# Kernel optimization log

Measured on AMD Instinct MI355X. Metric: run time of the kernel, lower is better.

Reference implementation:

```python
import jax, jax.numpy as jnp
import numpy as np

D_MODEL = 1024
N_HEADS = 16
HEAD_DIM = D_MODEL // N_HEADS
BASE = 10000.0


def _rope_cos_sin(seq_len):
    # inv_freq: [head_dim/2]
    inv_freq = 1.0 / (BASE ** (jnp.arange(0, HEAD_DIM, 2, dtype=jnp.float32) / HEAD_DIM))
    t = jnp.arange(seq_len, dtype=jnp.float32)
    freqs = jnp.outer(t, inv_freq)                 # [S, head_dim/2]
    emb = jnp.concatenate([freqs, freqs], axis=-1)  # [S, head_dim]
    return jnp.cos(emb), jnp.sin(emb)


def _rotate_half(x):
    x1, x2 = jnp.split(x, 2, axis=-1)
    return jnp.concatenate([-x2, x1], axis=-1)


def setup_inputs() -> dict:
    key = jax.random.key(0)
    ks = jax.random.split(key, 9)
    B, S, D = 2, 2048, D_MODEL
    sc = 1.0 / np.sqrt(D)
    return {
        "x": jax.random.normal(ks[0], (B, S, D), jnp.float32),
        "Wq": jax.random.normal(ks[1], (D, D), jnp.float32) * sc,
        "bq": jax.random.normal(ks[2], (D,), jnp.float32) * 0.01,
        "Wk": jax.random.normal(ks[3], (D, D), jnp.float32) * sc,
        "bk": jax.random.normal(ks[4], (D,), jnp.float32) * 0.01,
        "Wv": jax.random.normal(ks[5], (D, D), jnp.float32) * sc,
        "bv": jax.random.normal(ks[6], (D,), jnp.float32) * 0.01,
        "Wo": jax.random.normal(ks[7], (D, D), jnp.float32) * sc,
        "bo": jax.random.normal(ks[8], (D,), jnp.float32) * 0.01,
    }


def reference(x, Wq, bq, Wk, bk, Wv, bv, Wo, bo):
    B, S, D = x.shape
    H, Hd = N_HEADS, HEAD_DIM
    # projections (torch Linear: x @ W.T + b), reshape to [B, H, S, Hd]
    def proj(W, b):
        y = jnp.einsum('bsd,ed->bse', x, W) + b
        return y.reshape(B, S, H, Hd).transpose(0, 2, 1, 3)
    q, k, v = proj(Wq, bq), proj(Wk, bk), proj(Wv, bv)
    cos, sin = _rope_cos_sin(S)            # [S, Hd]
    cos = cos[None, None]                   # [1,1,S,Hd]
    sin = sin[None, None]
    q = q * cos + _rotate_half(q) * sin
    k = k * cos + _rotate_half(k) * sin
    scale = jnp.sqrt(jnp.float32(Hd))
    scores = jnp.einsum('bhqd,bhkd->bhqk', q, k) / scale  # [B,H,S,S]
    attn = jax.nn.softmax(scores, axis=-1)
    out = jnp.einsum('bhqk,bhkd->bhqd', attn, v)          # [B,H,S,Hd]
    out = out.transpose(0, 2, 1, 3).reshape(B, S, D)
    return jnp.einsum('bsd,ed->bse', out, Wo) + bo
```

## Files before the change

kernel.cpp:

```cpp
#include <hip/hip_runtime.h>
#include <hip/hip_fp16.h>
#include <math.h>

#define D_MODEL 1024
#define NH 16
#define HD 64
#define SEQ 2048
#define BATCH 2
#define MROWS (BATCH*SEQ)
#define KDIM 1024

typedef unsigned short u16;
typedef __attribute__((ext_vector_type(8))) _Float16 h8;
typedef __attribute__((ext_vector_type(8))) short s8v;
typedef __attribute__((ext_vector_type(4))) float f4v;

#define MFMAH(a, b, c) __builtin_amdgcn_mfma_f32_16x16x32_f16(a, b, c, 0, 0, 0)

__device__ __forceinline__ void gld16(const u16* g, u16* l) {
    __builtin_amdgcn_global_load_lds(
        (const __attribute__((address_space(1))) void*)g,
        (__attribute__((address_space(3))) void*)l, 16, 0, 0);
}

__device__ __forceinline__ u16 f32_to_f16(float f) {
    return __half_as_ushort(__float2half(f));
}

__global__ __launch_bounds__(256)
void convert_f16(const float* __restrict__ x,
                 const float* __restrict__ Wq, const float* __restrict__ Wk,
                 const float* __restrict__ Wv, const float* __restrict__ Wo,
                 u16* __restrict__ xF,
                 u16* __restrict__ WqF, u16* __restrict__ WkF,
                 u16* __restrict__ WvF, u16* __restrict__ WoF,
                 float2* __restrict__ ropeT) {
    int i = blockIdx.x * 256 + threadIdx.x;
    if (i >= (1 << 20)) {
        int idx2 = i - (1 << 20);
        int s  = idx2 >> 5;
        int dd = idx2 & 31;
        float inv = __expf(-(float)dd * 0.2878231366f);
        float ang = (float)s * inv;
        ropeT[idx2] = make_float2(cosf(ang), sinf(ang));
        return;
    }
    const float* src;
    u16* dst;
    int idx;
    if (i < (1 << 19)) {
        src = x; dst = xF; idx = i;
    } else {
        int j = i - (1 << 19);
        int w = j >> 17;
        idx = j & ((1 << 17) - 1);
        switch (w) {
            case 0:  src = Wq; dst = WqF; break;
            case 1:  src = Wk; dst = WkF; break;
            case 2:  src = Wv; dst = WvF; break;
            default: src = Wo; dst = WoF; break;
        }
    }
    float4 a = ((const float4*)src)[idx * 2];
    float4 b = ((const float4*)src)[idx * 2 + 1];
    s8v o;
    o[0] = (short)f32_to_f16(a.x); o[1] = (short)f32_to_f16(a.y);
    o[2] = (short)f32_to_f16(a.z); o[3] = (short)f32_to_f16(a.w);
    o[4] = (short)f32_to_f16(b.x); o[5] = (short)f32_to_f16(b.y);
    o[6] = (short)f32_to_f16(b.z); o[7] = (short)f32_to_f16(b.w);
    ((s8v*)dst)[idx] = o;
}

__global__ __launch_bounds__(256, 2)
void qkv_gemm(const u16* __restrict__ xF, const u16* __restrict__ WqF,
              const u16* __restrict__ WkF, const u16* __restrict__ WvF,
              const float* __restrict__ bq, const float* __restrict__ bk,
              const float* __restrict__ bv,
              const float2* __restrict__ ropeT,
              u16* __restrict__ QF, u16* __restrict__ KF,
              u16* __restrict__ VtF, float* __restrict__ km2) {
    __shared__ __align__(16) u16 SMEM[32768];

    const int t    = threadIdx.x;
    const int w    = t >> 6;
    const int lane = t & 63;
    const int quad = lane >> 4;
    const int l15  = lane & 15;
    const int wr   = w >> 1;
    const int wc   = w & 1;

    const int bid  = blockIdx.x;
    const int xcd  = bid & 7;
    const int j    = bid >> 3;
    const int m0   = (xcd * 4 + (j & 3)) * 128;
    const int yt   = j >> 2;
    const int wsel = yt >> 3;
    const int n0   = (yt & 7) * 128;

    const u16* Bg;
    const float* bias;
    if (wsel == 0)      { Bg = WqF; bias = bq; }
    else if (wsel == 1) { Bg = WkF; bias = bk; }
    else                { Bg = WvF; bias = bv; }

    const int lr = lane >> 3;
    const int lc = (((lane & 7) ^ lr)) * 8;

    f4v acc[4][4];
    #pragma unroll
    for (int i = 0; i < 4; i++)
        #pragma unroll
        for (int jj = 0; jj < 4; jj++)
            acc[i][jj] = (f4v){0.f, 0.f, 0.f, 0.f};

#define STAGE(K0, DB) do {                                                   \
    u16* As_ = SMEM + (DB);                                                  \
    u16* Bs_ = As_ + 8192;                                                   \
    _Pragma("unroll")                                                        \
    for (int jj_ = 0; jj_ < 4; jj_++) {                                      \
        int seg = jj_ * 4 + w;                                               \
        gld16(xF + (size_t)(m0 + seg * 8 + lr) * KDIM + (K0) + lc,           \
              As_ + seg * 512);                                              \
        gld16(Bg + (size_t)(n0 + seg * 8 + lr) * KDIM + (K0) + lc,           \
              Bs_ + seg * 512);                                              \
    }                                                                        \
} while (0)

    STAGE(0, 0);
    __syncthreads();

    int buf = 0;
    for (int k0 = 0; k0 < KDIM; k0 += 64) {
        if (k0 + 64 < KDIM) STAGE(k0 + 64, (buf ^ 1) * 16384);

        const u16* As = SMEM + buf * 16384;
        const u16* Bs = As + 8192;
        #pragma unroll
        for (int kk = 0; kk < 2; kk++) {
            const int swz = ((kk * 4 + quad) ^ (l15 & 7)) << 3;
            h8 a[4], b[4];
            #pragma unroll
            for (int mt = 0; mt < 4; mt++)
                a[mt] = *(const h8*)&As[(wr * 64 + mt * 16 + l15) * 64 + swz];
            #pragma unroll
            for (int nt = 0; nt < 4; nt++)
                b[nt] = *(const h8*)&Bs[(wc * 64 + nt * 16 + l15) * 64 + swz];
            #pragma unroll
            for (int mt = 0; mt < 4; mt++)
                #pragma unroll
                for (int nt = 0; nt < 4; nt++)
                    acc[mt][nt] = MFMAH(a[mt], b[nt], acc[mt][nt]);
        }
        __syncthreads();
        buf ^= 1;
    }
#undef STAGE

    const int bb = m0 >> 11;
    const int s0 = m0 & 2047;
    const int h0 = n0 >> 6;

    if (wsel < 2) {
        u16* OF = (wsel == 0) ? QF : KF;
        float kn_max = 0.f;
        #pragma unroll
        for (int mt = 0; mt < 4; mt++) {
            #pragma unroll
            for (int r = 0; r < 4; r++) {
                int R = wr * 64 + mt * 16 + quad * 4 + r;
                int s = s0 + R;
                float rowsum = 0.f;
                #pragma unroll
                for (int nt = 0; nt < 2; nt++) {
                    int col = wc * 64 + nt * 16 + l15;
                    int n1 = n0 + col;
                    int dd = n1 & 31;
                    float v1 = acc[mt][nt][r]     + bias[n1];
                    float v2 = acc[mt][nt + 2][r] + bias[n1 + 32];
                    float2 cssn = ropeT[(s << 5) | dd];
                    float cs  = cssn.x;
                    float sn  = cssn.y;
                    float r1 = v1 * cs - v2 * sn;
                    float r2 = v2 * cs + v1 * sn;
                    rowsum += v1 * v1 + v2 * v2;
                    SMEM[R * 128 + (((col >> 3) ^ (R & 15)) << 3) + (col & 7)]
                        = f32_to_f16(r1);
                    int col2 = col + 32;
                    SMEM[R * 128 + (((col2 >> 3) ^ (R & 15)) << 3) + (col2 & 7)]
                        = f32_to_f16(r2);
                }
                if (wsel == 1) {
                    rowsum += __shfl_xor(rowsum, 1, 64);
                    rowsum += __shfl_xor(rowsum, 2, 64);
                    rowsum += __shfl_xor(rowsum, 4, 64);
                    rowsum += __shfl_xor(rowsum, 8, 64);
                    kn_max = fmaxf(kn_max, rowsum);
                }
            }
        }
        if (wsel == 1) {
            kn_max = fmaxf(kn_max, __shfl_xor(kn_max, 16, 64));
            kn_max = fmaxf(kn_max, __shfl_xor(kn_max, 32, 64));
            if (lane == 0) atomicMax((int*)km2, __float_as_int(kn_max));
        }
        __syncthreads();
        #pragma unroll
        for (int cc = 0; cc < 8; cc++) {
            int idx  = cc * 256 + t;
            int hl   = idx >> 10;
            int rem  = idx & 1023;
            int R    = rem >> 3;
            int dch  = rem & 7;
            s8v val = *(const s8v*)&SMEM[R * 128 +
                          (((hl * 8 + dch) ^ (R & 15)) << 3)];
            *(s8v*)(OF + (((size_t)bb * NH + h0 + hl) * SEQ + s0 + R) * 64
                       + dch * 8) = val;
        }
    } else {
        #pragma unroll
        for (int mt = 0; mt < 4; mt++) {
            #pragma unroll
            for (int nt = 0; nt < 4; nt++) {
                int n = wc * 64 + nt * 16 + l15;
                float bv_ = bias[n0 + n];
                #pragma unroll
                for (int r = 0; r < 4; r++) {
                    int m = wr * 64 + mt * 16 + quad * 4 + r;
                    float v = acc[mt][nt][r] + bv_;
                    SMEM[n * 128 + (((m >> 3) ^ (n & 15)) << 3) + (m & 7)]
                        = f32_to_f16(v);
                }
            }
        }
        __syncthreads();
        #pragma unroll
        for (int cc = 0; cc < 8; cc++) {
            int idx = cc * 256 + t;
            int n   = idx >> 4;
            int mc  = idx & 15;
            int d   = n & 63;
            int hh  = n >> 6;
            size_t obase = ((size_t)((bb * NH + h0 + hh) * HD + d)) * SEQ + s0;
            s8v val = *(const s8v*)&SMEM[n * 128 + ((mc ^ (n & 15)) << 3)];
            *(s8v*)(VtF + obase + mc * 8) = val;
        }
    }
}

__global__ __launch_bounds__(256, 4)
void flash_attn(const u16* __restrict__ QF, const u16* __restrict__ KF,
                const u16* __restrict__ VtF,
                const float* __restrict__ kmax2,
                u16* __restrict__ AOF) {
    __shared__ __align__(16) u16 KS[2][32 * 72];
    __shared__ __align__(16) u16 VtS[2][64 * 40];
    __shared__ __align__(16) u16 PS[64 * 40];

    const int t    = threadIdx.x;
    const int w    = t >> 6;
    const int lane = t & 63;
    const int quad = lane >> 4;
    const int l15  = lane & 15;

    const int bid = blockIdx.x;
    const int xcd = bid & 7;
    const int j   = bid >> 3;
    const int bh  = xcd * 4 + (j & 3);
    const int q0  = (j >> 2) * 64;

    const size_t kvbase = (size_t)bh * SEQ * HD;
    const float km2 = kmax2[0];

    h8 qf[2];
    float mb[4];
    {
        const u16* qp = QF + kvbase +
            (size_t)(q0 + w * 16 + l15) * HD + quad * 8;
        qf[0] = *(const h8*)qp;
        qf[1] = *(const h8*)(qp + 32);
        float qn2 = 0.f;
        #pragma unroll
        for (int st = 0; st < 2; st++)
            #pragma unroll
            for (int e = 0; e < 8; e++) {
                float v = (float)qf[st][e];
                qn2 += v * v;
            }
        qn2 += __shfl_xor(qn2, 16, 64);
        qn2 += __shfl_xor(qn2, 32, 64);
        #pragma unroll
        for (int r = 0; r < 4; r++) {
            int src = (lane & 48) | (quad * 4 + r);
            float qr = __shfl(qn2, src, 64);
            mb[r] = sqrtf(qr * km2) * 0.125f;
        }
    }

    f4v o[4];
    float lsum[4];
    #pragma unroll
    for (int nt = 0; nt < 4; nt++) {
        o[nt] = (f4v){0.f, 0.f, 0.f, 0.f};
        lsum[nt] = 0.f;
    }

    for (int k0 = 0; k0 < SEQ; k0 += 64) {
        __syncthreads();

        {
            int row = t >> 3;
            int dc  = (t & 7) * 8;
            *(s8v*)&KS[0][row * 72 + dc] =
                *(const s8v*)(KF + kvbase + (size_t)(k0 + row) * HD + dc);
            *(s8v*)&KS[1][row * 72 + dc] =
                *(const s8v*)(KF + kvbase + (size_t)(k0 + 32 + row) * HD + dc);
        }
        {
            int d  = t >> 2;
            int kc = (t & 3) * 8;
            size_t g = (size_t)bh * HD * SEQ + (size_t)d * SEQ + k0 + kc;
            int col = kc ^ (((d >> 3) & 3) << 3);
            *(s8v*)&VtS[0][d * 40 + col] = *(const s8v*)(VtF + g);
            *(s8v*)&VtS[1][d * 40 + col] = *(const s8v*)(VtF + g + 32);
        }
        __syncthreads();

        #pragma unroll
        for (int sub = 0; sub < 2; sub++) {
            const u16* kb0 = KS[sub] + l15 * 72 + quad * 8;
            const u16* kb1 = KS[sub] + (16 + l15) * 72 + quad * 8;
            h8 kh0 = *(const h8*)kb0, kh1 = *(const h8*)(kb0 + 32);
            h8 kh2 = *(const h8*)kb1, kh3 = *(const h8*)(kb1 + 32);

            f4v sc0 = (f4v){0.f, 0.f, 0.f, 0.f};
            f4v sc1 = (f4v){0.f, 0.f, 0.f, 0.f};
            sc0 = MFMAH(qf[0], kh0, sc0);
            sc0 = MFMAH(qf[1], kh1, sc0);
            sc1 = MFMAH(qf[0], kh2, sc1);
            sc1 = MFMAH(qf[1], kh3, sc1);

            #pragma unroll
            for (int r = 0; r < 4; r++) {
                float p0 = __expf(sc0[r] * 0.125f - mb[r]);
                float p1 = __expf(sc1[r] * 0.125f - mb[r]);
                lsum[r] += p0 + p1;
                int row_l = w * 16 + quad * 4 + r;
                int cs = row_l & 8;
                PS[row_l * 40 + (l15 ^ cs)]        = f32_to_f16(p0);
                PS[row_l * 40 + ((16 + l15) ^ cs)] = f32_to_f16(p1);
            }

            const int prow = w * 16 + l15;
            h8 ph = *(const h8*)&PS[prow * 40 + ((quad * 8) ^ (prow & 8))];
            #pragma unroll
            for (int nt = 0; nt < 4; nt++) {
                int dim = nt * 16 + l15;
                int voff = dim * 40 + ((quad * 8) ^ (((dim >> 3) & 3) << 3));
                o[nt] = MFMAH(ph, *(const h8*)&VtS[sub][voff], o[nt]);
            }
        }
    }

    const int b = bh >> 4;
    const int h = bh & 15;
    #pragma unroll
    for (int r = 0; r < 4; r++) {
        float l = lsum[r];
        l += __shfl_xor(l, 1, 64);
        l += __shfl_xor(l, 2, 64);
        l += __shfl_xor(l, 4, 64);
        l += __shfl_xor(l, 8, 64);
        float inv_l = 1.0f / l;
        int s = q0 + w * 16 + quad * 4 + r;
        size_t obase = (((size_t)b * SEQ + s) * NH + h) * HD;
        #pragma unroll
        for (int nt = 0; nt < 4; nt++) {
            AOF[obase + nt * 16 + l15] = f32_to_f16(o[nt][r] * inv_l);
        }
    }
}

__global__ __launch_bounds__(256, 2)
void gemm_out(const u16* __restrict__ AF, const u16* __restrict__ BF,
              const float* __restrict__ bias, float* __restrict__ out) {
    __shared__ __align__(16) u16 SMEM[24576];

    const int t    = threadIdx.x;
    const int w    = t >> 6;
    const int lane = t & 63;
    const int quad = lane >> 4;
    const int l15  = lane & 15;
    const int wr   = w >> 1;
    const int wc   = w & 1;

    const int bid = blockIdx.x;
    const int xcd = bid & 7;
    const int j   = bid >> 3;
    const int m0  = (xcd * 4 + (j & 3)) * 128;
    const int n0  = (j >> 2) * 64;

    const int lr = lane >> 3;
    const int lc = (((lane & 7) ^ lr)) * 8;

    f4v acc[4][2];
    #pragma unroll
    for (int i = 0; i < 4; i++)
        #pragma unroll
        for (int jj = 0; jj < 2; jj++)
            acc[i][jj] = (f4v){0.f, 0.f, 0.f, 0.f};

#define STAGE(K0, DB) do {                                                   \
    u16* As_ = SMEM + (DB);                                                  \
    u16* Bs_ = As_ + 8192;                                                   \
    _Pragma("unroll")                                                        \
    for (int jj_ = 0; jj_ < 4; jj_++) {                                      \
        int seg = jj_ * 4 + w;                                               \
        gld16(AF + (size_t)(m0 + seg * 8 + lr) * KDIM + (K0) + lc,           \
              As_ + seg * 512);                                              \
    }                                                                        \
    _Pragma("unroll")                                                        \
    for (int jj_ = 0; jj_ < 2; jj_++) {                                      \
        int seg = jj_ * 4 + w;                                               \
        gld16(BF + (size_t)(n0 + seg * 8 + lr) * KDIM + (K0) + lc,           \
              Bs_ + seg * 512);                                              \
    }                                                                        \
} while (0)

    STAGE(0, 0);
    __syncthreads();

    int buf = 0;
    for (int k0 = 0; k0 < KDIM; k0 += 64) {
        if (k0 + 64 < KDIM) STAGE(k0 + 64, (buf ^ 1) * 12288);

        const u16* As = SMEM + buf * 12288;
        const u16* Bs = As + 8192;
        #pragma unroll
        for (int kk = 0; kk < 2; kk++) {
            const int swz = ((kk * 4 + quad) ^ (l15 & 7)) << 3;
            h8 a[4], b[2];
            #pragma unroll
            for (int mt = 0; mt < 4; mt++)
                a[mt] = *(const h8*)&As[(wr * 64 + mt * 16 + l15) * 64 + swz];
            #pragma unroll
            for (int nt = 0; nt < 2; nt++)
                b[nt] = *(const h8*)&Bs[(wc * 32 + nt * 16 + l15) * 64 + swz];
            #pragma unroll
            for (int mt = 0; mt < 4; mt++)
                #pragma unroll
                for (int nt = 0; nt < 2; nt++)
                    acc[mt][nt] = MFMAH(a[mt], b[nt], acc[mt][nt]);
        }
        __syncthreads();
        buf ^= 1;
    }
#undef STAGE

    #pragma unroll
    for (int mt = 0; mt < 4; mt++) {
        #pragma unroll
        for (int nt = 0; nt < 2; nt++) {
            int n = n0 + wc * 32 + nt * 16 + l15;
            float bv = bias[n];
            #pragma unroll
            for (int r = 0; r < 4; r++) {
                int m = m0 + wr * 64 + mt * 16 + quad * 4 + r;
                out[(size_t)m * 1024 + n] = acc[mt][nt][r] + bv;
            }
        }
    }
}

extern "C" void kernel_launch(void* const* d_in, const int* in_sizes, int n_in,
                              void* d_out, int out_size, void* d_ws, size_t ws_size,
                              hipStream_t stream) {
    const float* x  = (const float*)d_in[0];
    const float* Wq = (const float*)d_in[1];
    const float* bq = (const float*)d_in[2];
    const float* Wk = (const float*)d_in[3];
    const float* bk = (const float*)d_in[4];
    const float* Wv = (const float*)d_in[5];
    const float* bv = (const float*)d_in[6];
    const float* Wo = (const float*)d_in[7];
    const float* bo = (const float*)d_in[8];
    float* out = (float*)d_out;

    const size_t TEN = (size_t)MROWS * KDIM;
    const size_t WSZ = (size_t)KDIM * KDIM;

    u16* xF  = (u16*)d_ws;
    u16* WqF = xF + TEN;
    u16* WkF = WqF + WSZ;
    u16* WvF = WkF + WSZ;
    u16* WoF = WvF + WSZ;
    u16* QF  = WoF + WSZ;
    u16* KF  = QF + TEN;
    u16* VtF = KF + TEN;
    float* km2 = (float*)(VtF + TEN);
    float2* ropeT = (float2*)(km2 + 4);
    u16* AOF = xF;

    convert_f16<<<4352, 256, 0, stream>>>(x, Wq, Wk, Wv, Wo,
                                          xF, WqF, WkF, WvF, WoF, ropeT);

    hipMemsetAsync(km2, 0, 4, stream);

    qkv_gemm<<<768, 256, 0, stream>>>(xF, WqF, WkF, WvF,
                                      bq, bk, bv, ropeT, QF, KF, VtF, km2);

    flash_attn<<<1024, 256, 0, stream>>>(QF, KF, VtF, km2, AOF);

    gemm_out<<<512, 256, 0, stream>>>(AOF, WoF, bo, out);
}
```

Before: 210.6 us.

## Prefetch next K/V tile into registers, raise MFMA priority, repad P buffer

The flash attention loop now issues global loads for the next K and Vt tile into registers right after storing the current tile to shared memory, so global latency overlaps with the current tile's compute. MFMA sections are wrapped in s_setprio to favour matrix issue across waves. The P staging buffer changes from a 40-halfword XOR-swizzled stride to a 36-halfword padded stride. This adds register pressure at 4 waves/SIMD occupancy, and the new P layout may change LDS bank-conflict behaviour for the 16-byte reads.

```diff
diff --git a/kernel.cpp b/kernel.cpp
--- a/kernel.cpp
+++ b/kernel.cpp
@@ -254,7 +254,7 @@
                 u16* __restrict__ AOF) {
     __shared__ __align__(16) u16 KS[2][32 * 72];
     __shared__ __align__(16) u16 VtS[2][64 * 40];
-    __shared__ __align__(16) u16 PS[64 * 40];
+    __shared__ __align__(16) u16 PS[64 * 36];
 
     const int t    = threadIdx.x;
     const int w    = t >> 6;
@@ -304,24 +304,31 @@
         lsum[nt] = 0.f;
     }
 
+    const int krow = t >> 3;
+    const int kdc  = (t & 7) * 8;
+    const u16* kgp = KF + kvbase + (size_t)krow * HD + kdc;
+    const int vd   = t >> 2;
+    const int vkc  = (t & 3) * 8;
+    const int vcol = vkc ^ (((vd >> 3) & 3) << 3);
+    const u16* vgp = VtF + (size_t)bh * HD * SEQ + (size_t)vd * SEQ + vkc;
+
+    s8v krg0 = *(const s8v*)(kgp);
+    s8v krg1 = *(const s8v*)(kgp + (size_t)32 * HD);
+    s8v vrg0 = *(const s8v*)(vgp);
+    s8v vrg1 = *(const s8v*)(vgp + 32);
+
     for (int k0 = 0; k0 < SEQ; k0 += 64) {
         __syncthreads();
-
-        {
-            int row = t >> 3;
-            int dc  = (t & 7) * 8;
-            *(s8v*)&KS[0][row * 72 + dc] =
-                *(const s8v*)(KF + kvbase + (size_t)(k0 + row) * HD + dc);
-            *(s8v*)&KS[1][row * 72 + dc] =
-                *(const s8v*)(KF + kvbase + (size_t)(k0 + 32 + row) * HD + dc);
-        }
-        {
-            int d  = t >> 2;
-            int kc = (t & 3) * 8;
-            size_t g = (size_t)bh * HD * SEQ + (size_t)d * SEQ + k0 + kc;
-            int col = kc ^ (((d >> 3) & 3) << 3);
-            *(s8v*)&VtS[0][d * 40 + col] = *(const s8v*)(VtF + g);
-            *(s8v*)&VtS[1][d * 40 + col] = *(const s8v*)(VtF + g + 32);
+        *(s8v*)&KS[0][krow * 72 + kdc] = krg0;
+        *(s8v*)&KS[1][krow * 72 + kdc] = krg1;
+        *(s8v*)&VtS[0][vd * 40 + vcol] = vrg0;
+        *(s8v*)&VtS[1][vd * 40 + vcol] = vrg1;
+        if (k0 + 64 < SEQ) {
+            const u16* kn = kgp + (size_t)(k0 + 64) * HD;
+            krg0 = *(const s8v*)(kn);
+            krg1 = *(const s8v*)(kn + (size_t)32 * HD);
+            vrg0 = *(const s8v*)(vgp + k0 + 64);
+            vrg1 = *(const s8v*)(vgp + k0 + 96);
         }
         __syncthreads();
 
@@ -334,10 +341,12 @@
 
             f4v sc0 = (f4v){0.f, 0.f, 0.f, 0.f};
             f4v sc1 = (f4v){0.f, 0.f, 0.f, 0.f};
+            __builtin_amdgcn_s_setprio(1);
             sc0 = MFMAH(qf[0], kh0, sc0);
             sc0 = MFMAH(qf[1], kh1, sc0);
             sc1 = MFMAH(qf[0], kh2, sc1);
             sc1 = MFMAH(qf[1], kh3, sc1);
+            __builtin_amdgcn_s_setprio(0);
 
             #pragma unroll
             for (int r = 0; r < 4; r++) {
@@ -345,19 +354,20 @@
                 float p1 = __expf(sc1[r] * 0.125f - mb[r]);
                 lsum[r] += p0 + p1;
                 int row_l = w * 16 + quad * 4 + r;
-                int cs = row_l & 8;
-                PS[row_l * 40 + (l15 ^ cs)]        = f32_to_f16(p0);
-                PS[row_l * 40 + ((16 + l15) ^ cs)] = f32_to_f16(p1);
+                PS[row_l * 36 + l15]      = f32_to_f16(p0);
+                PS[row_l * 36 + 16 + l15] = f32_to_f16(p1);
             }
 
             const int prow = w * 16 + l15;
-            h8 ph = *(const h8*)&PS[prow * 40 + ((quad * 8) ^ (prow & 8))];
+            h8 ph = *(const h8*)&PS[prow * 36 + quad * 8];
+            __builtin_amdgcn_s_setprio(1);
             #pragma unroll
             for (int nt = 0; nt < 4; nt++) {
                 int dim = nt * 16 + l15;
                 int voff = dim * 40 + ((quad * 8) ^ (((dim >> 3) & 3) << 3));
                 o[nt] = MFMAH(ph, *(const h8*)&VtS[sub][voff], o[nt]);
             }
+            __builtin_amdgcn_s_setprio(0);
         }
     }
 
```

New measurement: 223.5 us. 6.1% more time.
